# Performance work log

Measured on AMD Instinct MI355X. Metric: run time of the kernel, lower is better.

Reference implementation:

```python
import jax, jax.numpy as jnp
import numpy as np

B, T, D = 2, 4096, 1024
H = 8
HD = D // H            # head_dim = 128
STRIDES = (1, 1, 2, 2, 4, 4, 8, 8)   # resolution_schedule
BANDS = 8              # spectral_bands
RH = 256               # router_hidden


def setup_inputs() -> dict:
    key = jax.random.key(0)
    ks = jax.random.split(key, 12)
    def xavier(k, shape):
        fan_in, fan_out = shape[-2], shape[-1]
        lim = 0.5 * (6.0 / (fan_in + fan_out)) ** 0.5   # gain=0.5 xavier_uniform
        return jax.random.uniform(k, shape, jnp.float32, -lim, lim)
    return {
        "x":          jax.random.normal(ks[0], (B, T, D), jnp.float32),
        "Wq":         xavier(ks[1], (H, D, HD)),
        "Wk":         xavier(ks[2], (H, D, HD)),
        "Wv":         xavier(ks[3], (H, D, HD)),
        "band_gates": jax.random.normal(ks[4], (H, BANDS), jnp.float32) * 0.1,
        "alphas":     jax.random.normal(ks[5], (H,), jnp.float32) * 0.1,
        "rW1":        xavier(ks[6], (D, RH)),
        "rb1":        jnp.zeros((RH,), jnp.float32),
        "rW2":        xavier(ks[7], (RH, H)),
        "rb2":        jnp.zeros((H,), jnp.float32),
        "Wout":       xavier(ks[8], (HD, D)),
    }


def _flux_head(x, Wq, Wk, Wv, band_gate, alpha, stride):
    # one FluxHead: strided K/V pooling + spectral logit gating + contra-flow residual
    q = jnp.einsum('btd,dh->bth', x, Wq)          # [B,T,HD]
    k = jnp.einsum('btd,dh->bth', x, Wk)
    v = jnp.einsum('btd,dh->bth', x, Wv)
    Tk = T // stride
    k = k.reshape(B, Tk, stride, HD).mean(axis=2)  # avg-pool K/V along time
    v = v.reshape(B, Tk, stride, HD).mean(axis=2)
    logits = jnp.einsum('bth,bkh->btk', q, k) / jnp.sqrt(jnp.float32(HD))  # [B,T,Tk]
    # spectral frequency gating on logits (rFFT over key axis, per-band sigmoid gain)
    F = jnp.fft.rfft(logits, axis=-1)              # [B,T,Tk//2+1] complex
    nbins = F.shape[-1]
    band_idx = jnp.clip((jnp.arange(nbins) * BANDS) // nbins, 0, BANDS - 1)
    gains = jax.nn.sigmoid(band_gate)[band_idx]    # [nbins]
    logits = jnp.fft.irfft(F * gains, n=Tk, axis=-1)
    attn = jax.nn.softmax(logits, axis=-1)
    out = jnp.einsum('btk,bkh->bth', attn, v)      # [B,T,HD]
    # contra-flow: reverse-sequence residual with learned gate
    return out + jnp.tanh(alpha) * out[:, ::-1, :]


def reference(x, Wq, Wk, Wv, band_gates, alphas, rW1, rb1, rW2, rb2, Wout):
    head_outs = [
        _flux_head(x, Wq[h], Wk[h], Wv[h], band_gates[h], alphas[h], STRIDES[h])
        for h in range(H)
    ]
    stacked = jnp.stack(head_outs, axis=2)                      # [B,T,H,HD]
    hid = jax.nn.relu(jnp.einsum('btd,dr->btr', x, rW1) + rb1)  # router MLP
    w = jax.nn.softmax(jnp.einsum('btr,rh->bth', hid, rW2) + rb2, axis=-1)
    mixed = jnp.einsum('bth,bthc->btc', w, stacked)             # [B,T,HD]
    return jnp.einsum('btc,cd->btd', mixed, Wout)               # [B,T,D]
```

## Files before the change

kernel.cpp:

```cpp
#include <hip/hip_runtime.h>
#include <hip/hip_bf16.h>

typedef __attribute__((ext_vector_type(8))) short short8;
typedef __attribute__((ext_vector_type(4))) short short4v;
typedef __attribute__((ext_vector_type(4))) float f32x4;
typedef unsigned short u16;

#define T_ 4096
#define D_ 1024
#define ISSL2E (0.08838834764831845f * 1.4426950408889634f)

__device__ __forceinline__ u16 f2bf(float f) {
  union { float f; unsigned u; } v; v.f = f;
  unsigned r = v.u + 0x7FFFu + ((v.u >> 16) & 1u);
  return (u16)(r >> 16);
}

__global__ __launch_bounds__(256) void pool_all(const float* __restrict__ x,
    u16* __restrict__ p1, u16* __restrict__ p2, u16* __restrict__ p4, u16* __restrict__ p8) {
  const int blk = blockIdx.x;
  const int b = blk >> 9, t0 = (blk & 511) << 3;
  const float* src = x + ((long)b * T_ + t0) * D_;
#pragma unroll
  for (int j = 0; j < 4; ++j) {
    const int c = threadIdx.x + j * 256;
    float v[8];
#pragma unroll
    for (int r = 0; r < 8; ++r) v[r] = src[r * D_ + c];
#pragma unroll
    for (int r = 0; r < 8; ++r) p1[((long)b * 4096 + t0 + r) * D_ + c] = f2bf(v[r]);
#pragma unroll
    for (int r = 0; r < 4; ++r)
      p2[((long)b * 2048 + (t0 >> 1) + r) * D_ + c] = f2bf((v[2*r] + v[2*r+1]) * 0.5f);
#pragma unroll
    for (int r = 0; r < 2; ++r)
      p4[((long)b * 1024 + (t0 >> 2) + r) * D_ + c] =
          f2bf((v[4*r] + v[4*r+1] + v[4*r+2] + v[4*r+3]) * 0.25f);
    p8[((long)b * 512 + (t0 >> 3)) * D_ + c] =
        f2bf((v[0]+v[1]+v[2]+v[3]+v[4]+v[5]+v[6]+v[7]) * 0.125f);
  }
}

__global__ __launch_bounds__(256) void wprep(const float* __restrict__ Wq,
    const float* __restrict__ Wk, const float* __restrict__ Wv,
    const float* __restrict__ rW1, const float* __restrict__ Wout,
    u16* __restrict__ wqT, u16* __restrict__ kvT, u16* __restrict__ rw1T, u16* __restrict__ woutT) {
  const int idx = blockIdx.x * 256 + threadIdx.x;
  if (idx < 1048576) {
    const int h = idx >> 17, wi = idx & 131071;
    const int c = wi >> 10, k = wi & 1023;
    wqT[idx] = f2bf(Wq[(long)h * 131072 + k * 128 + c]);
  } else if (idx < 3145728) {
    const int lid = idx - 1048576;
    const int g = lid >> 19, wi = lid & 524287;
    const int n = wi >> 10, k = wi & 1023;
    const int kv = n >> 8, hh = (n >> 7) & 1, c = n & 127;
    const float* W = kv ? Wv : Wk;
    kvT[lid] = f2bf(W[(long)(2 * g + hh) * 131072 + k * 128 + c]);
  } else if (idx < 3407872) {
    const int lid = idx - 3145728;
    const int n = lid >> 10, k = lid & 1023;
    rw1T[lid] = f2bf(rW1[(long)k * 256 + n]);
  } else if (idx < 3538944) {
    const int lid = idx - 3407872;
    const int n = lid >> 7, k = lid & 127;
    woutT[lid] = f2bf(Wout[(long)k * 1024 + n]);
  }
}

__global__ __launch_bounds__(256) void tpose_all(const u16* __restrict__ KV,
                                                 u16* __restrict__ KT, u16* __restrict__ VT) {
  const int xt = blockIdx.x;
  int g, lx;
  if (xt < 128)      { g = 0; lx = xt; }
  else if (xt < 192) { g = 1; lx = xt - 128; }
  else if (xt < 224) { g = 2; lx = xt - 192; }
  else               { g = 3; lx = xt - 224; }
  const int Tk = 4096 >> g;
  const long kvrow[4] = {0, 8192, 12288, 14336};
  const long ktoff[4] = {0, 2097152, 3145728, 3670016};
  __shared__ u16 tile[32][33];
  const int z = blockIdx.z;
  const int b = z & 1, hh = (z >> 1) & 1, kv = z >> 2;
  const u16* src = KV + kvrow[g] * 512 + (long)b * Tk * 512 + kv * 256 + hh * 128;
  u16* dst = (kv ? VT : KT) + ktoff[g] + (long)(hh * 2 + b) * 128 * Tk;
  const int r0 = lx * 32, c0 = blockIdx.y * 32;
  const int ci = threadIdx.x & 31, ri = threadIdx.x >> 5;
#pragma unroll
  for (int j = 0; j < 4; ++j)
    tile[ri + 8 * j][ci] = src[(long)(r0 + ri + 8 * j) * 512 + c0 + ci];
  __syncthreads();
  const int key = r0 + ci;
  const int col = kv ? ((key & ~63) | (((key >> 4) & 1) << 5) | (((key >> 2) & 3) << 3)
                                    | (((key >> 5) & 1) << 2) | (key & 3))
                     : key;
#pragma unroll
  for (int j = 0; j < 4; ++j)
    dst[(long)(c0 + ri + 8 * j) * Tk + col] = tile[ci][ri + 8 * j];
}

__global__ __launch_bounds__(256) void irfft_c(const float* __restrict__ bg, u16* __restrict__ crep) {
  const int h = blockIdx.y;
  const int Tk = 4096 >> (h >> 1);
  const int mask = Tk - 1;
  if ((int)(blockIdx.x * 256) >= Tk) return;
  const int nb = (Tk >> 1) + 1;
  __shared__ float ct[4096];
  __shared__ float wm[2049];
  const int tid = threadIdx.x;
  const float w0 = 6.283185307179586f / (float)Tk;
  for (int j = tid; j < Tk; j += 256) ct[j] = cosf(w0 * (float)j);
  for (int m = tid; m < nb; m += 256) {
    int band = (m * 8) / nb; if (band > 7) band = 7;
    const float g = 1.f / (1.f + expf(-bg[h * 8 + band]));
    const float sc = (m == 0 || m == nb - 1) ? 1.f : 2.f;
    wm[m] = g * sc / (float)Tk;
  }
  __syncthreads();
  const int n = blockIdx.x * 256 + tid;
  float acc = 0.f;
  int idx = 0;
  for (int m = 0; m < nb; ++m) {
    acc += wm[m] * ct[idx];
    idx += n;
    if (idx >= Tk) idx -= Tk;
  }
  const u16 bf = f2bf(acc);
  u16* hb = crep + (long)h * 16416;
#pragma unroll
  for (int p = 0; p < 4; ++p) {
    const int q = (n - p) & mask;
    hb[p * 4104 + q] = bf;
    if (q < 8) hb[p * 4104 + q + Tk] = bf;
  }
}

__device__ __forceinline__ void gll16(const void* g, void* l) {
  __builtin_amdgcn_global_load_lds((const __attribute__((address_space(1))) void*)g,
                                   (__attribute__((address_space(3))) void*)l, 16, 0, 0);
}

__device__ __forceinline__ void gemm_core(const u16* __restrict__ A, const u16* __restrict__ Bt,
    void* __restrict__ Cv, int K, int lda, int ldb, int ldc, int tm, int tn, float alpha,
    bool obf, u16 (*lds)[2][128][32]) {
  const int tid = threadIdx.x, lane = tid & 63, wid = tid >> 6;
  const int wr = wid >> 1, wc = wid & 1;
  const int srow = lane >> 2;
  const int scol = ((lane & 3) ^ ((lane >> 3) & 3)) * 8;
  const u16* ga0 = A + (long)(tm + 32 * wid + srow) * lda + scol;
  const u16* ga1 = ga0 + (long)16 * lda;
  const u16* gb0 = Bt + (long)(tn + 32 * wid + srow) * ldb + scol;
  const u16* gb1 = gb0 + (long)16 * ldb;
  f32x4 acc[4][4] = {};
  const int nk = K >> 5;
  gll16(ga0, &lds[0][0][32 * wid][0]);
  gll16(ga1, &lds[0][0][32 * wid + 16][0]);
  gll16(gb0, &lds[0][1][32 * wid][0]);
  gll16(gb1, &lds[0][1][32 * wid + 16][0]);
  int buf = 0;
  const int fr = lane & 15;
  const int fo2 = (((lane >> 4) & 3) ^ ((lane >> 1) & 3)) * 8;
  for (int kt = 0; kt < nk; ++kt) {
    __syncthreads();
    if (kt + 1 < nk) {
      const long ko = (long)(kt + 1) * 32;
      gll16(ga0 + ko, &lds[buf ^ 1][0][32 * wid][0]);
      gll16(ga1 + ko, &lds[buf ^ 1][0][32 * wid + 16][0]);
      gll16(gb0 + ko, &lds[buf ^ 1][1][32 * wid][0]);
      gll16(gb1 + ko, &lds[buf ^ 1][1][32 * wid + 16][0]);
    }
    short8 af[4], bfr[4];
#pragma unroll
    for (int i = 0; i < 4; ++i) {
      af[i]  = *(const short8*)&lds[buf][0][wr * 64 + i * 16 + fr][fo2];
      bfr[i] = *(const short8*)&lds[buf][1][wc * 64 + i * 16 + fr][fo2];
    }
#pragma unroll
    for (int i = 0; i < 4; ++i)
#pragma unroll
      for (int j = 0; j < 4; ++j)
        acc[i][j] = __builtin_amdgcn_mfma_f32_16x16x32_bf16(af[i], bfr[j], acc[i][j], 0, 0, 0);
    buf ^= 1;
  }
  const int er = (lane >> 4) * 4, ec = lane & 15;
  if (obf) {
    u16* C = (u16*)Cv;
#pragma unroll
    for (int i = 0; i < 4; ++i)
#pragma unroll
      for (int j = 0; j < 4; ++j)
#pragma unroll
        for (int r = 0; r < 4; ++r)
          C[(long)(tm + wr * 64 + i * 16 + er + r) * ldc + (tn + wc * 64 + j * 16 + ec)] =
              f2bf(acc[i][j][r] * alpha);
  } else {
    float* C = (float*)Cv;
#pragma unroll
    for (int i = 0; i < 4; ++i)
#pragma unroll
      for (int j = 0; j < 4; ++j)
#pragma unroll
        for (int r = 0; r < 4; ++r)
          C[(long)(tm + wr * 64 + i * 16 + er + r) * ldc + (tn + wc * 64 + j * 16 + ec)] =
              acc[i][j][r] * alpha;
  }
}

template <bool OBF>
__global__ __launch_bounds__(256) void gemm_bt(const u16* __restrict__ A, const u16* __restrict__ Bt,
                                               void* __restrict__ Cv, int K, int lda, int ldb, int ldc,
                                               long abs_, long bbs, long cbs, float alpha) {
  __shared__ u16 lds[2][2][128][32];
  const u16* Az = A + (long)blockIdx.z * abs_;
  const u16* Bz = Bt + (long)blockIdx.z * bbs;
  void* Cz = OBF ? (void*)((u16*)Cv + (long)blockIdx.z * cbs)
                 : (void*)((float*)Cv + (long)blockIdx.z * cbs);
  gemm_core(Az, Bz, Cz, K, lda, ldb, ldc, blockIdx.x * 128, blockIdx.y * 128, alpha, OBF, lds);
}

__global__ __launch_bounds__(256) void gemm_p1(const u16* __restrict__ xbf,
    const u16* __restrict__ wqT, const u16* __restrict__ kvT, const u16* __restrict__ rw1T,
    u16* __restrict__ Qb, u16* __restrict__ KV, float* __restrict__ hid) {
  __shared__ u16 lds[2][2][128][32];
  const int id = blockIdx.x;
  if (id < 512) {
    gemm_core(xbf, wqT, Qb, 1024, 1024, 1024, 1024,
              (id >> 3) * 128, (id & 7) * 128, 1.f, true, lds);
  } else if (id < 992) {
    const int lid = id - 512;
    const int rt = lid >> 2, y = lid & 3;
    int g, lr;
    if (rt < 64)       { g = 0; lr = rt; }
    else if (rt < 96)  { g = 1; lr = rt - 64; }
    else if (rt < 112) { g = 2; lr = rt - 96; }
    else               { g = 3; lr = rt - 112; }
    const long xofs[4] = {0, 8388608, 12582912, 14680064};
    const long kvrow[4] = {0, 8192, 12288, 14336};
    gemm_core(xbf + xofs[g], kvT + (long)g * 524288, KV + kvrow[g] * 512,
              1024, 1024, 1024, 512, lr * 128, y * 128, 1.f, true, lds);
  } else {
    const int lid = id - 992;
    gemm_core(xbf, rw1T, hid, 1024, 1024, 1024, 256,
              (lid >> 1) * 128, (lid & 1) * 128, 1.f, false, lds);
  }
}

__global__ __launch_bounds__(256) void conv_k(const u16* __restrict__ crep,
    const u16* __restrict__ KT, u16* __restrict__ Kp) {
  const int z = blockIdx.z, h = z >> 1, b = z & 1, g = h >> 1;
  const int Tk = 4096 >> g, mask = Tk - 1;
  const int tm = blockIdx.x << 7;
  if (tm >= Tk) return;
  __shared__ u16 clds[16416];
  __shared__ u16 blds[2][4][128][32];
  const int tid = threadIdx.x, lane = tid & 63, wid = tid >> 6;
  const int wr = wid >> 1, wc = wid & 1;
  const int srow = lane >> 2;
  const int scol = ((lane & 3) ^ ((lane >> 3) & 3)) * 8;
  const int fr = lane & 15, fo = (lane >> 4) * 8;
  const int fo2 = (((lane >> 4) & 3) ^ ((lane >> 1) & 3)) * 8;
  {
    const short8* src = (const short8*)(crep + (long)h * 16416);
    short8* dst = (short8*)clds;
    for (int j = tid; j < 2052; j += 256) dst[j] = src[j];
  }
  const long ktofs = 4194304 - (4194304 >> g);
  const u16* Bt = KT + ktofs + (long)((h & 1) * 2 + b) * 128 * Tk;
  u16* out = Kp + ktofs + ((long)(h & 1) << 8) * Tk + ((long)b << 7) * Tk;
  const u16* gb0 = Bt + (long)(32 * wid + srow) * Tk + scol;
  const u16* gb1 = gb0 + (long)16 * Tk;
  f32x4 acc[4][4] = {};
  int base[4];
#pragma unroll
  for (int i = 0; i < 4; ++i) base[i] = (fo - (tm + wr * 64 + i * 16 + fr)) & mask;
  const int p = base[0] & 3;
  const u16* crow = clds + p * 4104;
  const int nk = Tk >> 7;
#pragma unroll
  for (int c = 0; c < 4; ++c) {
    gll16(gb0 + c * 32, &blds[0][c][32 * wid][0]);
    gll16(gb1 + c * 32, &blds[0][c][32 * wid + 16][0]);
  }
  int buf = 0;
  for (int kt = 0; kt < nk; ++kt) {
    __syncthreads();
    if (kt + 1 < nk) {
      const long ko = (long)(kt + 1) * 128;
#pragma unroll
      for (int c = 0; c < 4; ++c) {
        gll16(gb0 + ko + c * 32, &blds[buf ^ 1][c][32 * wid][0]);
        gll16(gb1 + ko + c * 32, &blds[buf ^ 1][c][32 * wid + 16][0]);
      }
    }
#pragma unroll
    for (int c = 0; c < 4; ++c) {
      short8 af[4], bfr[4];
#pragma unroll
      for (int i = 0; i < 4; ++i) {
        const int a0 = base[i] ^ p;
        short4v lo = *(const short4v*)(crow + a0);
        short4v hi = *(const short4v*)(crow + a0 + 4);
        af[i][0] = lo[0]; af[i][1] = lo[1]; af[i][2] = lo[2]; af[i][3] = lo[3];
        af[i][4] = hi[0]; af[i][5] = hi[1]; af[i][6] = hi[2]; af[i][7] = hi[3];
        base[i] = (base[i] + 32) & mask;
        bfr[i] = *(const short8*)&blds[buf][c][wc * 64 + i * 16 + fr][fo2];
      }
#pragma unroll
      for (int i = 0; i < 4; ++i)
#pragma unroll
        for (int j = 0; j < 4; ++j)
          acc[i][j] = __builtin_amdgcn_mfma_f32_16x16x32_bf16(af[i], bfr[j], acc[i][j], 0, 0, 0);
    }
    buf ^= 1;
  }
  const int er = (lane >> 4) * 4, ec = lane & 15;
#pragma unroll
  for (int i = 0; i < 4; ++i)
#pragma unroll
    for (int j = 0; j < 4; ++j)
#pragma unroll
      for (int r = 0; r < 4; ++r)
        out[(long)(tm + wr * 64 + i * 16 + er + r) * 128 + (wc * 64 + j * 16 + ec)] =
            f2bf(acc[i][j][r] * ISSL2E);
}

__global__ __launch_bounds__(256, 2) void flash(const u16* __restrict__ Qb,
    const u16* __restrict__ Kp, const u16* __restrict__ VT, float* __restrict__ O) {
  const int wg = blockIdx.x;
  const int x = wg & 7, s = wg >> 3;
  const int t4 = s >> 4;
  const int lvl = t4 ^ (t4 >> 1);
  const int hh = x >> 2, b = (x >> 1) & 1;
  const int h = lvl * 2 + hh;
  const int qtm = (((x & 1) << 4) + (s & 15)) << 7;
  const int Tk = 4096 >> lvl;
  const int nt = Tk >> 6;

  __shared__ __align__(16) char smem[65536];
  u16 (*Kl)[4][64][32] = (u16(*)[4][64][32])smem;
  u16 (*Vl)[128][64]   = (u16(*)[128][64])(smem + 32768);

  const int tid = threadIdx.x, lane = tid & 63, wid = tid >> 6;
  const int fr = lane & 15, gs = lane >> 4;
  const int fo = gs * 8;
  const int fo2 = ((gs & 3) ^ ((lane >> 1) & 3)) * 8;

  const long ktofs = 4194304 - (4194304 >> lvl);
  const u16* kbase = Kp + ktofs + (long)(hh * 2 + b) * 128 * Tk;
  const u16* vbase = VT + ktofs + (long)(hh * 2 + b) * 128 * Tk;

  short8 aq[2][4];
#pragma unroll
  for (int m = 0; m < 2; ++m)
#pragma unroll
    for (int kk = 0; kk < 4; ++kk)
      aq[m][kk] = *(const short8*)(Qb +
          ((long)(b * 4096 + qtm + wid * 32 + m * 16 + fr)) * 1024 + h * 128 + kk * 32 + fo);

  const u16* kptr = kbase + (long)(lane >> 2) * 128 + wid * 32 +
                    (((lane & 3) ^ ((lane >> 3) & 3)) << 3);
  const u16* vptr = vbase + (long)(32 * wid + (lane >> 3)) * Tk +
                    (((lane & 7) ^ ((lane >> 3) & 7)) << 3);

  const char* kbL  = smem + fr * 64 + fo2 * 2;
  const char* vbL0 = smem + 32768 + fr * 128 + ((((gs    ) ^ (fr & 7)) & 7) << 4);
  const char* vbL1 = smem + 32768 + fr * 128 + ((((gs ^ 4) ^ (fr & 7)) & 7) << 4);

  f32x4 acc[2][8] = {};
  f32x4 accl[2] = {};
  float mr[2] = {-3e38f, -3e38f};

  short8 ones;
#pragma unroll
  for (int i = 0; i < 8; ++i) ones[i] = (short)0x3F80;

#pragma unroll
  for (int i = 0; i < 4; ++i) {
    gll16(kptr + i * 2048, &Kl[0][wid][i * 16][0]);
    gll16(vptr + (long)i * 8 * Tk, &Vl[0][32 * wid + 8 * i][0]);
  }

  int cur = 0;
  for (int kt = 0; kt < nt; ++kt) {
    asm volatile("s_waitcnt vmcnt(0)" ::: "memory");
    __builtin_amdgcn_sched_barrier(0);
    __builtin_amdgcn_s_barrier();
    __builtin_amdgcn_sched_barrier(0);
    if (kt + 1 < nt) {
      const int ktn = kt + 1;
#pragma unroll
      for (int i = 0; i < 4; ++i) {
        gll16(kptr + (long)ktn * 8192 + i * 2048, &Kl[cur ^ 1][wid][i * 16][0]);
        gll16(vptr + (long)ktn * 64 + (long)i * 8 * Tk, &Vl[cur ^ 1][32 * wid + 8 * i][0]);
      }
    }
    const char* kc = kbL + cur * 16384;
    f32x4 sa[2][4] = {};
    __builtin_amdgcn_s_setprio(1);
#pragma unroll
    for (int kk = 0; kk < 4; ++kk) {
      short8 bk[4];
#pragma unroll
      for (int jm = 0; jm < 4; ++jm)
        bk[jm] = *(const short8*)(kc + kk * 4096 + jm * 1024);
#pragma unroll
      for (int m = 0; m < 2; ++m)
#pragma unroll
        for (int jm = 0; jm < 4; ++jm)
          sa[m][jm] = __builtin_amdgcn_mfma_f32_16x16x32_bf16(bk[jm], aq[m][kk], sa[m][jm], 0, 0, 0);
    }
    __builtin_amdgcn_s_setprio(0);
    float tmx[2];
#pragma unroll
    for (int m = 0; m < 2; ++m) {
      float v0 = fmaxf(fmaxf(sa[m][0][0], sa[m][0][1]), fmaxf(sa[m][0][2], sa[m][0][3]));
      float v1 = fmaxf(fmaxf(sa[m][1][0], sa[m][1][1]), fmaxf(sa[m][1][2], sa[m][1][3]));
      float v2 = fmaxf(fmaxf(sa[m][2][0], sa[m][2][1]), fmaxf(sa[m][2][2], sa[m][2][3]));
      float v3 = fmaxf(fmaxf(sa[m][3][0], sa[m][3][1]), fmaxf(sa[m][3][2], sa[m][3][3]));
      float v = fmaxf(fmaxf(v0, v1), fmaxf(v2, v3));
      v = fmaxf(v, __shfl_xor(v, 16));
      v = fmaxf(v, __shfl_xor(v, 32));
      tmx[m] = v;
    }
    const bool need = (tmx[0] > mr[0] + 8.f) | (tmx[1] > mr[1] + 8.f);
    if (__any((int)need)) {
#pragma unroll
      for (int m = 0; m < 2; ++m) {
        const float mn = fmaxf(mr[m], tmx[m]);
        const float av = __builtin_amdgcn_exp2f(mr[m] - mn);
        mr[m] = mn;
#pragma unroll
        for (int jd = 0; jd < 8; ++jd)
#pragma unroll
          for (int r = 0; r < 4; ++r) acc[m][jd][r] *= av;
#pragma unroll
        for (int r = 0; r < 4; ++r) accl[m][r] *= av;
      }
    }
#pragma unroll
    for (int m = 0; m < 2; ++m)
#pragma unroll
      for (int jm = 0; jm < 4; ++jm)
#pragma unroll
        for (int r = 0; r < 4; ++r)
          sa[m][jm][r] = __builtin_amdgcn_exp2f(sa[m][jm][r] - mr[m]);
    unsigned pk[2][4][2];
#pragma unroll
    for (int m = 0; m < 2; ++m)
#pragma unroll
      for (int jm = 0; jm < 4; ++jm) {
        asm("v_cvt_pk_bf16_f32 %0, %1, %2" : "=v"(pk[m][jm][0]) : "v"(sa[m][jm][0]), "v"(sa[m][jm][1]));
        asm("v_cvt_pk_bf16_f32 %0, %1, %2" : "=v"(pk[m][jm][1]) : "v"(sa[m][jm][2]), "v"(sa[m][jm][3]));
      }
    const char* vc0 = vbL0 + cur * 16384;
    const char* vc1 = vbL1 + cur * 16384;
    __builtin_amdgcn_s_setprio(1);
#pragma unroll
    for (int kk = 0; kk < 2; ++kk) {
      short8 pt[2];
#pragma unroll
      for (int m = 0; m < 2; ++m) {
        union { unsigned u[4]; short8 s; } pp;
        pp.u[0] = pk[m][kk][0];     pp.u[1] = pk[m][kk][1];
        pp.u[2] = pk[m][kk + 2][0]; pp.u[3] = pk[m][kk + 2][1];
        pt[m] = pp.s;
      }
      const char* vc = kk ? vc1 : vc0;
#pragma unroll
      for (int jd = 0; jd < 8; ++jd) {
        short8 bb = *(const short8*)(vc + jd * 2048);
#pragma unroll
        for (int m = 0; m < 2; ++m)
          acc[m][jd] = __builtin_amdgcn_mfma_f32_16x16x32_bf16(bb, pt[m], acc[m][jd], 0, 0, 0);
      }
#pragma unroll
      for (int m = 0; m < 2; ++m)
        accl[m] = __builtin_amdgcn_mfma_f32_16x16x32_bf16(ones, pt[m], accl[m], 0, 0, 0);
    }
    __builtin_amdgcn_s_setprio(0);
    cur ^= 1;
  }
  __syncthreads();
  float* Ot = (float*)smem;
  float* ot = Ot + wid * 16 * 132;
#pragma unroll
  for (int m = 0; m < 2; ++m) {
    const float inv = 1.f / accl[m][0];
#pragma unroll
    for (int jd = 0; jd < 8; ++jd) {
      f32x4 v;
#pragma unroll
      for (int r = 0; r < 4; ++r) v[r] = acc[m][jd][r] * inv;
      *(f32x4*)&ot[fr * 132 + jd * 16 + gs * 4] = v;
    }
    asm volatile("s_waitcnt lgkmcnt(0)" ::: "memory");
    __builtin_amdgcn_sched_barrier(0);
    const int q = qtm + wid * 32 + m * 16 + (lane >> 2);
    float* od = O + ((long)(b * 4096 + q) * 8 + h) * 128 + (lane & 3) * 32;
#pragma unroll
    for (int j = 0; j < 8; ++j) {
      f32x4 v = *(const f32x4*)&ot[(lane >> 2) * 132 + (lane & 3) * 32 + j * 4];
      *(f32x4*)&od[j * 4] = v;
    }
    asm volatile("s_waitcnt lgkmcnt(0)" ::: "memory");
    __builtin_amdgcn_sched_barrier(0);
  }
}

__global__ __launch_bounds__(256) void router_mix(const float* __restrict__ hid,
    const float* __restrict__ rb1, const float* __restrict__ rW2, const float* __restrict__ rb2,
    const float* __restrict__ al, const float* __restrict__ O, u16* __restrict__ mixed) {
  const int tok = blockIdx.x;
  const int b = tok >> 12, t = tok & 4095;
  const int tid = threadIdx.x;
  __shared__ float lred[4][8];
  __shared__ float wgt[8];
  __shared__ float ta[8];
  const float hv = fmaxf(hid[(long)tok * 256 + tid] + rb1[tid], 0.f);
  const float4* w4 = (const float4*)(rW2 + tid * 8);
  const float4 wa = w4[0], wb = w4[1];
  float part[8] = {hv * wa.x, hv * wa.y, hv * wa.z, hv * wa.w,
                   hv * wb.x, hv * wb.y, hv * wb.z, hv * wb.w};
#pragma unroll
  for (int h = 0; h < 8; ++h) {
    float v = part[h];
#pragma unroll
    for (int o = 1; o < 64; o <<= 1) v += __shfl_xor(v, o);
    if ((tid & 63) == 0) lred[tid >> 6][h] = v;
  }
  __syncthreads();
  if (tid < 8) ta[tid] = tanhf(al[tid]);
  if (tid == 0) {
    float lg[8], m = -1e30f;
#pragma unroll
    for (int h = 0; h < 8; ++h) {
      lg[h] = lred[0][h] + lred[1][h] + lred[2][h] + lred[3][h] + rb2[h];
      m = fmaxf(m, lg[h]);
    }
    float s = 0.f;
#pragma unroll
    for (int h = 0; h < 8; ++h) { lg[h] = __expf(lg[h] - m); s += lg[h]; }
    const float inv = 1.f / s;
#pragma unroll
    for (int h = 0; h < 8; ++h) wgt[h] = lg[h] * inv;
  }
  __syncthreads();
  if (tid < 128) {
    const long base = (long)tok * 1024 + tid;
    const long rbase = ((long)b * 4096 + (4095 - t)) * 1024 + tid;
    float acc = 0.f;
#pragma unroll
    for (int h = 0; h < 8; ++h)
      acc += wgt[h] * (O[base + h * 128] + ta[h] * O[rbase + h * 128]);
    mixed[(long)tok * 128 + tid] = f2bf(acc);
  }
}

extern "C" void kernel_launch(void* const* d_in, const int* in_sizes, int n_in,
                              void* d_out, int out_size, void* d_ws, size_t ws_size,
                              hipStream_t stream) {
  const float* x    = (const float*)d_in[0];
  const float* Wq   = (const float*)d_in[1];
  const float* Wk   = (const float*)d_in[2];
  const float* Wv   = (const float*)d_in[3];
  const float* bg   = (const float*)d_in[4];
  const float* al   = (const float*)d_in[5];
  const float* rW1  = (const float*)d_in[6];
  const float* rb1  = (const float*)d_in[7];
  const float* rW2  = (const float*)d_in[8];
  const float* rb2  = (const float*)d_in[9];
  const float* Wout = (const float*)d_in[10];
  float* out = (float*)d_out;

  const size_t MB = 1u << 20;
  char* w = (char*)d_ws;
  u16*   xbf   = (u16*)(w + 0);
  float* O     = (float*)(w + 0);
  u16*   Qb    = (u16*)(w + 32 * MB);
  u16*   KV    = (u16*)(w + 48 * MB);
  u16*   Kp    = (u16*)(w + 48 * MB);
  u16*   KT    = (u16*)(w + 63 * MB);
  u16*   VT    = (u16*)(w + 70 * MB + 512 * 1024);
  float* hid   = (float*)(w + 78 * MB);
  u16*   wqT   = (u16*)(w + 86 * MB);
  u16*   kvT   = (u16*)(w + 88 * MB);
  u16*   rw1T  = (u16*)(w + 92 * MB);
  u16*   woutT = (u16*)(w + 92 * MB + 512 * 1024);
  u16*   crep  = (u16*)(w + 92 * MB + 768 * 1024);
  u16*   mixed = (u16*)(w + 93 * MB + 512 * 1024);
  u16*   xp2   = (u16*)(w + 16 * MB);
  u16*   xp4   = (u16*)(w + 24 * MB);
  u16*   xp8   = (u16*)(w + 28 * MB);

  pool_all<<<dim3(1024), dim3(256), 0, stream>>>(x, xbf, xp2, xp4, xp8);
  wprep<<<dim3(13824), dim3(256), 0, stream>>>(Wq, Wk, Wv, rW1, Wout, wqT, kvT, rw1T, woutT);

  gemm_p1<<<dim3(1120), dim3(256), 0, stream>>>(xbf, wqT, kvT, rw1T, Qb, KV, hid);

  tpose_all<<<dim3(240, 4, 8), dim3(256), 0, stream>>>(KV, KT, VT);
  irfft_c<<<dim3(16, 8), dim3(256), 0, stream>>>(bg, crep);

  conv_k<<<dim3(32, 1, 16), dim3(256), 0, stream>>>(crep, KT, Kp);

  flash<<<dim3(512), dim3(256), 0, stream>>>(Qb, Kp, VT, O);

  router_mix<<<dim3(8192), dim3(256), 0, stream>>>(hid, rb1, rW2, rb2, al, O, mixed);
  gemm_bt<false><<<dim3(64, 8), dim3(256), 0, stream>>>(mixed, woutT, out,
      128, 128, 128, 1024, 0, 0, 0, 1.f);
}
```

Before: 328.5 us.

## Split flash attention over two key halves and merge with a combine kernel

The flash kernel now splits each query tile's key range into two halves, doubling the grid to 1024 workgroups. Each half writes unnormalized partial outputs plus per-row max and sum, and a new ocombine kernel merges them with log-sum-exp weights. V is now single-buffered in LDS with an extra barrier, which cuts LDS to 48KB, and the workspace layout is reorganized. This targets poor occupancy and load imbalance across the 256 CUs, at the cost of extra partial-output traffic, an added kernel launch, and less V prefetch overlap.

Measured after the change: 372.0 us. 1.13x slower.

```diff
diff --git a/kernel.cpp b/kernel.cpp
--- a/kernel.cpp
+++ b/kernel.cpp
@@ -324,21 +324,23 @@
             f2bf(acc[i][j][r] * ISSL2E);
 }
 
-__global__ __launch_bounds__(256, 2) void flash(const u16* __restrict__ Qb,
-    const u16* __restrict__ Kp, const u16* __restrict__ VT, float* __restrict__ O) {
+__global__ __launch_bounds__(256) void flash(const u16* __restrict__ Qb,
+    const u16* __restrict__ Kp, const u16* __restrict__ VT,
+    float* __restrict__ Op, float* __restrict__ mlb) {
   const int wg = blockIdx.x;
   const int x = wg & 7, s = wg >> 3;
-  const int t4 = s >> 4;
-  const int lvl = t4 ^ (t4 >> 1);
-  const int hh = x >> 2, b = (x >> 1) & 1;
+  const int t5 = s >> 5;
+  const int lvl = t5 ^ (t5 >> 1);
+  const int hh = x >> 2, b = (x >> 1) & 1, kh = x & 1;
   const int h = lvl * 2 + hh;
-  const int qtm = (((x & 1) << 4) + (s & 15)) << 7;
-  const int Tk = 4096 >> lvl;
-  const int nt = Tk >> 6;
-
-  __shared__ __align__(16) char smem[65536];
+  const int qtm = (s & 31) << 7;
+  const int Tkf = 4096 >> lvl;
+  const int Tk2 = Tkf >> 1;
+  const int nt = Tk2 >> 6;
+
+  __shared__ __align__(16) char smem[49152];
   u16 (*Kl)[4][64][32] = (u16(*)[4][64][32])smem;
-  u16 (*Vl)[128][64]   = (u16(*)[128][64])(smem + 32768);
+  u16 (*Vl)[64]        = (u16(*)[64])(smem + 32768);
 
   const int tid = threadIdx.x, lane = tid & 63, wid = tid >> 6;
   const int fr = lane & 15, gs = lane >> 4;
@@ -346,8 +348,8 @@
   const int fo2 = ((gs & 3) ^ ((lane >> 1) & 3)) * 8;
 
   const long ktofs = 4194304 - (4194304 >> lvl);
-  const u16* kbase = Kp + ktofs + (long)(hh * 2 + b) * 128 * Tk;
-  const u16* vbase = VT + ktofs + (long)(hh * 2 + b) * 128 * Tk;
+  const u16* kbase = Kp + ktofs + (long)(hh * 2 + b) * 128 * Tkf + (long)kh * Tk2 * 128;
+  const u16* vbase = VT + ktofs + (long)(hh * 2 + b) * 128 * Tkf;
 
   short8 aq[2][4];
 #pragma unroll
@@ -359,7 +361,7 @@
 
   const u16* kptr = kbase + (long)(lane >> 2) * 128 + wid * 32 +
                     (((lane & 3) ^ ((lane >> 3) & 3)) << 3);
-  const u16* vptr = vbase + (long)(32 * wid + (lane >> 3)) * Tk +
+  const u16* vptr = vbase + (long)(32 * wid + (lane >> 3)) * Tkf + kh * Tk2 +
                     (((lane & 7) ^ ((lane >> 3) & 7)) << 3);
 
   const char* kbL  = smem + fr * 64 + fo2 * 2;
@@ -375,10 +377,7 @@
   for (int i = 0; i < 8; ++i) ones[i] = (short)0x3F80;
 
 #pragma unroll
-  for (int i = 0; i < 4; ++i) {
-    gll16(kptr + i * 2048, &Kl[0][wid][i * 16][0]);
-    gll16(vptr + (long)i * 8 * Tk, &Vl[0][32 * wid + 8 * i][0]);
-  }
+  for (int i = 0; i < 4; ++i) gll16(kptr + i * 2048, &Kl[0][wid][i * 16][0]);
 
   int cur = 0;
   for (int kt = 0; kt < nt; ++kt) {
@@ -386,13 +385,13 @@
     __builtin_amdgcn_sched_barrier(0);
     __builtin_amdgcn_s_barrier();
     __builtin_amdgcn_sched_barrier(0);
+#pragma unroll
+    for (int i = 0; i < 4; ++i)
+      gll16(vptr + (long)kt * 64 + (long)i * 8 * Tkf, &Vl[32 * wid + 8 * i][0]);
     if (kt + 1 < nt) {
-      const int ktn = kt + 1;
-#pragma unroll
-      for (int i = 0; i < 4; ++i) {
-        gll16(kptr + (long)ktn * 8192 + i * 2048, &Kl[cur ^ 1][wid][i * 16][0]);
-        gll16(vptr + (long)ktn * 64 + (long)i * 8 * Tk, &Vl[cur ^ 1][32 * wid + 8 * i][0]);
-      }
+#pragma unroll
+      for (int i = 0; i < 4; ++i)
+        gll16(kptr + (long)(kt + 1) * 8192 + i * 2048, &Kl[cur ^ 1][wid][i * 16][0]);
     }
     const char* kc = kbL + cur * 16384;
     f32x4 sa[2][4] = {};
@@ -452,8 +451,11 @@
         asm("v_cvt_pk_bf16_f32 %0, %1, %2" : "=v"(pk[m][jm][0]) : "v"(sa[m][jm][0]), "v"(sa[m][jm][1]));
         asm("v_cvt_pk_bf16_f32 %0, %1, %2" : "=v"(pk[m][jm][1]) : "v"(sa[m][jm][2]), "v"(sa[m][jm][3]));
       }
-    const char* vc0 = vbL0 + cur * 16384;
-    const char* vc1 = vbL1 + cur * 16384;
+    if (kt + 1 < nt) { asm volatile("s_waitcnt vmcnt(4)" ::: "memory"); }
+    else             { asm volatile("s_waitcnt vmcnt(0)" ::: "memory"); }
+    __builtin_amdgcn_sched_barrier(0);
+    __builtin_amdgcn_s_barrier();
+    __builtin_amdgcn_sched_barrier(0);
     __builtin_amdgcn_s_setprio(1);
 #pragma unroll
     for (int kk = 0; kk < 2; ++kk) {
@@ -465,7 +467,7 @@
         pp.u[2] = pk[m][kk + 2][0]; pp.u[3] = pk[m][kk + 2][1];
         pt[m] = pp.s;
       }
-      const char* vc = kk ? vc1 : vc0;
+      const char* vc = kk ? vbL1 : vbL0;
 #pragma unroll
       for (int jd = 0; jd < 8; ++jd) {
         short8 bb = *(const short8*)(vc + jd * 2048);
@@ -483,20 +485,20 @@
   __syncthreads();
   float* Ot = (float*)smem;
   float* ot = Ot + wid * 16 * 132;
+  float* Obase = Op + (long)kh * 8388608;
 #pragma unroll
   for (int m = 0; m < 2; ++m) {
-    const float inv = 1.f / accl[m][0];
 #pragma unroll
     for (int jd = 0; jd < 8; ++jd) {
       f32x4 v;
 #pragma unroll
-      for (int r = 0; r < 4; ++r) v[r] = acc[m][jd][r] * inv;
+      for (int r = 0; r < 4; ++r) v[r] = acc[m][jd][r];
       *(f32x4*)&ot[fr * 132 + jd * 16 + gs * 4] = v;
     }
     asm volatile("s_waitcnt lgkmcnt(0)" ::: "memory");
     __builtin_amdgcn_sched_barrier(0);
     const int q = qtm + wid * 32 + m * 16 + (lane >> 2);
-    float* od = O + ((long)(b * 4096 + q) * 8 + h) * 128 + (lane & 3) * 32;
+    float* od = Obase + ((long)(b * 4096 + q) * 8 + h) * 128 + (lane & 3) * 32;
 #pragma unroll
     for (int j = 0; j < 8; ++j) {
       f32x4 v = *(const f32x4*)&ot[(lane >> 2) * 132 + (lane & 3) * 32 + j * 4];
@@ -504,7 +506,38 @@
     }
     asm volatile("s_waitcnt lgkmcnt(0)" ::: "memory");
     __builtin_amdgcn_sched_barrier(0);
-  }
+    if (gs == 0) {
+      const int q2 = qtm + wid * 32 + m * 16 + fr;
+      ((float2*)mlb)[(long)kh * 65536 + (long)(b * 4096 + q2) * 8 + h] =
+          make_float2(mr[m], accl[m][0]);
+    }
+  }
+}
+
+__global__ __launch_bounds__(256) void ocombine(float* __restrict__ Op, const float* __restrict__ mlb) {
+  const int tok = blockIdx.x;
+  const int tid = threadIdx.x;
+  __shared__ float e[8][2];
+  if (tid < 8) {
+    const float2 a = ((const float2*)mlb)[(long)tok * 8 + tid];
+    const float2 c = ((const float2*)mlb)[65536 + (long)tok * 8 + tid];
+    const float M = fmaxf(a.x, c.x);
+    const float w1 = exp2f(a.x - M), w2 = exp2f(c.x - M);
+    const float inv = 1.f / (w1 * a.y + w2 * c.y);
+    e[tid][0] = w1 * inv;
+    e[tid][1] = w2 * inv;
+  }
+  __syncthreads();
+  const int h = tid >> 5, d4 = (tid & 31) << 2;
+  float* p0 = Op + (long)tok * 1024 + h * 128 + d4;
+  const float* p1 = p0 + 8388608;
+  f32x4 o1 = *(f32x4*)p0;
+  f32x4 o2 = *(const f32x4*)p1;
+  const float e1 = e[h][0], e2 = e[h][1];
+  f32x4 r;
+#pragma unroll
+  for (int i = 0; i < 4; ++i) r[i] = o1[i] * e1 + o2[i] * e2;
+  *(f32x4*)p0 = r;
 }
 
 __global__ __launch_bounds__(256) void router_mix(const float* __restrict__ hid,
@@ -574,23 +607,24 @@
 
   const size_t MB = 1u << 20;
   char* w = (char*)d_ws;
+  float* Opart = (float*)(w);
+  float* mlbuf = (float*)(w + 64 * MB);
+  u16*   Kp    = (u16*)(w + 66 * MB);
+  u16*   KT    = (u16*)(w + 74 * MB);
+  u16*   VT    = (u16*)(w + 82 * MB);
+  u16*   Qb    = (u16*)(w + 90 * MB);
+  float* hid   = (float*)(w + 106 * MB);
+  u16*   wqT   = (u16*)(w + 114 * MB);
+  u16*   kvT   = (u16*)(w + 116 * MB);
+  u16*   rw1T  = (u16*)(w + 120 * MB);
+  u16*   woutT = (u16*)(w + 120 * MB + 512 * 1024);
+  u16*   crep  = (u16*)(w + 121 * MB);
+  u16*   mixed = (u16*)(w + 122 * MB);
   u16*   xbf   = (u16*)(w + 0);
-  float* O     = (float*)(w + 0);
-  u16*   Qb    = (u16*)(w + 32 * MB);
-  u16*   KV    = (u16*)(w + 48 * MB);
-  u16*   Kp    = (u16*)(w + 48 * MB);
-  u16*   KT    = (u16*)(w + 63 * MB);
-  u16*   VT    = (u16*)(w + 70 * MB + 512 * 1024);
-  float* hid   = (float*)(w + 78 * MB);
-  u16*   wqT   = (u16*)(w + 86 * MB);
-  u16*   kvT   = (u16*)(w + 88 * MB);
-  u16*   rw1T  = (u16*)(w + 92 * MB);
-  u16*   woutT = (u16*)(w + 92 * MB + 512 * 1024);
-  u16*   crep  = (u16*)(w + 92 * MB + 768 * 1024);
-  u16*   mixed = (u16*)(w + 93 * MB + 512 * 1024);
   u16*   xp2   = (u16*)(w + 16 * MB);
   u16*   xp4   = (u16*)(w + 24 * MB);
   u16*   xp8   = (u16*)(w + 28 * MB);
+  u16*   KV    = (u16*)(w + 30 * MB);
 
   pool_all<<<dim3(1024), dim3(256), 0, stream>>>(x, xbf, xp2, xp4, xp8);
   wprep<<<dim3(13824), dim3(256), 0, stream>>>(Wq, Wk, Wv, rW1, Wout, wqT, kvT, rw1T, woutT);
@@ -602,9 +636,10 @@
 
   conv_k<<<dim3(32, 1, 16), dim3(256), 0, stream>>>(crep, KT, Kp);
 
-  flash<<<dim3(512), dim3(256), 0, stream>>>(Qb, Kp, VT, O);
-
-  router_mix<<<dim3(8192), dim3(256), 0, stream>>>(hid, rb1, rW2, rb2, al, O, mixed);
+  flash<<<dim3(1024), dim3(256), 0, stream>>>(Qb, Kp, VT, Opart, mlbuf);
+  ocombine<<<dim3(8192), dim3(256), 0, stream>>>(Opart, mlbuf);
+
+  router_mix<<<dim3(8192), dim3(256), 0, stream>>>(hid, rb1, rW2, rb2, al, Opart, mixed);
   gemm_bt<false><<<dim3(64, 8), dim3(256), 0, stream>>>(mixed, woutT, out,
       128, 128, 128, 1024, 0, 0, 0, 1.f);
 }
```
